# Kernel tuning notes

Measured on AMD Instinct MI355X. Metric: run time of the kernel, lower is better.

## Reference

```python
import jax, jax.numpy as jnp
import numpy as np

B, C, T, F = 4, 96, 320, 256
BN_EPS = 1e-5


def _cbp(x, W, b, gamma, beta, mean, var, a):
    """1x1 Conv2d + BatchNorm2d (inference stats) + PReLU (single param)."""
    y = jnp.einsum('oc,bctf->botf', W, x) + b[None, :, None, None]
    scale = gamma * jax.lax.rsqrt(var + BN_EPS)
    y = (y - mean[None, :, None, None]) * scale[None, :, None, None] + beta[None, :, None, None]
    return jnp.where(y >= 0, y, a * y)


def setup_inputs() -> dict:
    key = jax.random.key(0)
    ks = jax.random.split(key, 24)
    d = {"inp": jax.random.normal(ks[0], (B, C, T, F), dtype=jnp.float32)}

    def mk_params(i, cout):
        kk = jax.random.split(ks[i], 7)
        return dict(
            W=jax.random.normal(kk[0], (cout, C), dtype=jnp.float32) / np.sqrt(C),
            b=jnp.zeros((cout,), dtype=jnp.float32),
            gamma=jnp.ones((cout,), dtype=jnp.float32) + 0.1 * jax.random.normal(kk[1], (cout,), dtype=jnp.float32),
            beta=0.1 * jax.random.normal(kk[2], (cout,), dtype=jnp.float32),
            mean=0.1 * jax.random.normal(kk[3], (cout,), dtype=jnp.float32),
            var=jax.random.uniform(kk[4], (cout,), dtype=jnp.float32) + 0.5,
            a=jnp.float32(0.25),
        )

    for tag, i, cout in (("f", 1, 3 * C), ("t", 2, 2 * C), ("p", 3, C)):
        p = mk_params(i, cout)
        for k, v in p.items():
            d[k + "_" + tag] = v
    return d


def reference(inp,
              W_f, b_f, gamma_f, beta_f, mean_f, var_f, a_f,
              W_t, b_t, gamma_t, beta_t, mean_t, var_t, a_t,
              W_p, b_p, gamma_p, beta_p, mean_p, var_p, a_p):
    c = inp.shape[1]
    scale = 1.0 / jnp.sqrt(jnp.float32(c))

    # frequency-axis attention
    f_qkv = _cbp(inp, W_f, b_f, gamma_f, beta_f, mean_f, var_f, a_f)  # [B,3C,T,F]
    qf, kf, v = f_qkv[:, :c], f_qkv[:, c:2 * c], f_qkv[:, 2 * c:]
    f_score = jnp.einsum('bctf,bcty->btfy', qf, kf) * scale
    f_score = jax.nn.softmax(f_score, axis=-1)
    f_out = jnp.einsum('btfy,bcty->bctf', f_score, v)

    # time-axis attention (NOTE: original's masked_fill is non-inplace and
    # its result is discarded, so the causal mask has NO effect; replicated.)
    t_qk = _cbp(inp, W_t, b_t, gamma_t, beta_t, mean_t, var_t, a_t)  # [B,2C,T,F]
    qt, kt = t_qk[:, :c], t_qk[:, c:]
    t_score = jnp.einsum('bctf,bcyf->bfty', qt, kt) * scale
    t_score = jax.nn.softmax(t_score, axis=-1)
    t_out = jnp.einsum('bfty,bcyf->bctf', t_score, f_out)

    out = _cbp(t_out, W_p, b_p, gamma_p, beta_p, mean_p, var_p, a_p)
    return out + inp
```

## Files before the change

### kernel.cpp

```cpp
#include <hip/hip_runtime.h>
#include <math.h>

typedef float f4 __attribute__((ext_vector_type(4)));
typedef float f2 __attribute__((ext_vector_type(2)));
typedef float f32x4 __attribute__((ext_vector_type(4)));
typedef _Float16 h8 __attribute__((ext_vector_type(8)));

constexpr int B_ = 4, C_ = 96, T_ = 320, F_ = 256;
constexpr int TF_ = T_ * F_;
constexpr float EPS_ = 1e-5f;
constexpr size_t QH_ = (size_t)C_ * TF_;

constexpr int WHF = 0, WLF = 27648, WHT = 55296, WLT = 73728,
              WHP = 92160, WLP = 101376, WTOT = 110592;

__global__ __launch_bounds__(256)
void prep_kernel(const float* __restrict__ Wf, const float* __restrict__ Wt,
                 const float* __restrict__ Wp,
                 const float* __restrict__ bf, const float* __restrict__ gf,
                 const float* __restrict__ bef, const float* __restrict__ mf,
                 const float* __restrict__ vf,
                 const float* __restrict__ bt, const float* __restrict__ gt,
                 const float* __restrict__ bet, const float* __restrict__ mt,
                 const float* __restrict__ vt,
                 const float* __restrict__ bp, const float* __restrict__ gp,
                 const float* __restrict__ bep, const float* __restrict__ mp,
                 const float* __restrict__ vp,
                 _Float16* __restrict__ wsp, float* __restrict__ scsh)
{
    const int gtid = blockIdx.x * 256 + threadIdx.x;
    const int gsz  = gridDim.x * 256;
    for (int i = gtid; i < 27648; i += gsz) {
        const float w = Wf[i]; const _Float16 h = (_Float16)w;
        wsp[WHF + i] = h; wsp[WLF + i] = (_Float16)(w - (float)h);
    }
    for (int i = gtid; i < 18432; i += gsz) {
        const float w = Wt[i]; const _Float16 h = (_Float16)w;
        wsp[WHT + i] = h; wsp[WLT + i] = (_Float16)(w - (float)h);
    }
    for (int i = gtid; i < 9216; i += gsz) {
        const float w = Wp[i]; const _Float16 h = (_Float16)w;
        wsp[WHP + i] = h; wsp[WLP + i] = (_Float16)(w - (float)h);
    }
    if (gtid < 288) {
        const float sc = gf[gtid] * rsqrtf(vf[gtid] + EPS_);
        scsh[2 * gtid] = sc;
        scsh[2 * gtid + 1] = fmaf(bf[gtid] - mf[gtid], sc, bef[gtid]);
    } else if (gtid < 480) {
        const int i = gtid - 288;
        const float sc = gt[i] * rsqrtf(vt[i] + EPS_);
        scsh[576 + 2 * i] = sc;
        scsh[576 + 2 * i + 1] = fmaf(bt[i] - mt[i], sc, bet[i]);
    } else if (gtid < 576) {
        const int i = gtid - 480;
        const float sc = gp[i] * rsqrtf(vp[i] + EPS_);
        scsh[960 + 2 * i] = sc;
        scsh[960 + 2 * i + 1] = fmaf(bp[i] - mp[i], sc, bep[i]);
    }
}

__global__ __launch_bounds__(256, 3)
void conv_ft(const float* __restrict__ x, const _Float16* __restrict__ wsp,
             const float* __restrict__ scsh,
             const float* __restrict__ aPf, const float* __restrict__ aPt,
             _Float16* __restrict__ yf, _Float16* __restrict__ yt,
             int bsx, int bsyf, int bsyt)
{
    constexpr int LS = 200;
    extern __shared__ _Float16 ldsh[];
    _Float16* Xs = ldsh;

    x  += (size_t)blockIdx.y * bsx;
    yf += (size_t)blockIdx.y * bsyf;
    yt += (size_t)blockIdx.y * bsyt;

    const int tid = threadIdx.x;
    const int p0  = blockIdx.x * 64;

    const float* xg = x + p0;
    for (int e = tid; e < 64 * 12; e += 256) {
        const int p = e & 63, k0 = (e >> 6) * 8;
        const float* xp = xg + (size_t)k0 * TF_ + p;
        h8 hv, lv;
#pragma unroll
        for (int j = 0; j < 8; ++j) {
            const float xv = xp[(size_t)j * TF_];
            const _Float16 xh = (_Float16)xv;
            hv[j] = xh;
            lv[j] = (_Float16)(xv - (float)xh);
        }
        *(h8*)&Xs[p * LS + k0]      = hv;
        *(h8*)&Xs[p * LS + 96 + k0] = lv;
    }

    const int lane = tid & 63, wid = tid >> 6;
    const int l16 = lane & 15, lg = lane >> 4;
    const int wm = wid >> 1, wn = wid & 1;
    const float af_ = aPf[0], at_ = aPt[0];
    __syncthreads();

#pragma unroll 1
    for (int cg = 0; cg < 5; ++cg) {
        const _Float16 *Wh, *Wl; const float* ss; float a; _Float16* yo;
        if (cg < 3) {
            Wh = wsp + WHF + cg * 9216;  Wl = wsp + WLF + cg * 9216;
            ss = scsh + cg * 192;        a = af_;
            yo = yf + (size_t)cg * QH_;
        } else {
            const int c2 = cg - 3;
            Wh = wsp + WHT + c2 * 9216;  Wl = wsp + WLT + c2 * 9216;
            ss = scsh + 576 + c2 * 192;  a = at_;
            yo = yt + (size_t)c2 * QH_;
        }

        f32x4 acc[3][2];
#pragma unroll
        for (int m = 0; m < 3; ++m)
#pragma unroll
            for (int n = 0; n < 2; ++n) acc[m][n] = (f32x4){0.f, 0.f, 0.f, 0.f};

#pragma unroll
        for (int kk = 0; kk < 3; ++kk) {
            h8 bfh[2], bfl[2];
#pragma unroll
            for (int n = 0; n < 2; ++n) {
                const int prow = (wn * 2 + n) * 16 + l16;
                bfh[n] = *(const h8*)&Xs[prow * LS + kk * 32 + lg * 8];
                bfl[n] = *(const h8*)&Xs[prow * LS + 96 + kk * 32 + lg * 8];
            }
#pragma unroll
            for (int m = 0; m < 3; ++m) {
                const int row = (wm * 3 + m) * 16 + l16;
                const h8 wh = *(const h8*)&Wh[row * 96 + kk * 32 + lg * 8];
                const h8 wl = *(const h8*)&Wl[row * 96 + kk * 32 + lg * 8];
#pragma unroll
                for (int n = 0; n < 2; ++n) {
                    acc[m][n] = __builtin_amdgcn_mfma_f32_16x16x32_f16(wh, bfh[n], acc[m][n], 0, 0, 0);
                    acc[m][n] = __builtin_amdgcn_mfma_f32_16x16x32_f16(wl, bfh[n], acc[m][n], 0, 0, 0);
                    acc[m][n] = __builtin_amdgcn_mfma_f32_16x16x32_f16(wh, bfl[n], acc[m][n], 0, 0, 0);
                }
            }
        }

#pragma unroll
        for (int m = 0; m < 3; ++m) {
#pragma unroll
            for (int r = 0; r < 4; ++r) {
                const int col = (wm * 3 + m) * 16 + lg * 4 + r;
                const f2 sp = *(const f2*)&ss[2 * col];
                _Float16* yr = yo + (size_t)col * TF_ + p0 + wn * 32 + l16;
#pragma unroll
                for (int n = 0; n < 2; ++n) {
                    const float v = fmaf(acc[m][n][r], sp[0], sp[1]);
                    yr[n * 16] = (_Float16)(v >= 0.f ? v : a * v);
                }
            }
        }
    }
}

__global__ __launch_bounds__(256, 3)
void conv_p(const _Float16* __restrict__ x, const _Float16* __restrict__ wsp,
            const float* __restrict__ scsh, const float* __restrict__ aPp,
            _Float16* __restrict__ y, int bsx, int bsy)
{
    constexpr int LS = 104, PT = 160, NN = 5;
    extern __shared__ _Float16 ldsh[];
    _Float16* Xs = ldsh;

    x += (size_t)blockIdx.y * bsx;
    y += (size_t)blockIdx.y * bsy;

    const int tid = threadIdx.x;
    const int pt  = blockIdx.x & 1;
    const int g   = blockIdx.x >> 1;
    const int p0  = pt * PT;

    const _Float16* xg = x + (size_t)g * 96 * T_ + p0;
    for (int e = tid; e < PT * 12; e += 256) {
        const int p = e % PT, k0 = (e / PT) * 8;
        const _Float16* xp = xg + (size_t)k0 * T_ + p;
        h8 hv;
#pragma unroll
        for (int j = 0; j < 8; ++j) hv[j] = xp[(size_t)j * T_];
        *(h8*)&Xs[p * LS + k0] = hv;
    }

    const int lane = tid & 63, wid = tid >> 6;
    const int l16 = lane & 15, lg = lane >> 4;
    const int wm = wid >> 1, wn = wid & 1;
    const float a = aPp[0];
    const _Float16* Wh = wsp + WHP;
    const _Float16* Wl = wsp + WLP;
    const float* ss = scsh + 960;
    __syncthreads();

    f32x4 acc[3][NN];
#pragma unroll
    for (int m = 0; m < 3; ++m)
#pragma unroll
        for (int n = 0; n < NN; ++n) acc[m][n] = (f32x4){0.f, 0.f, 0.f, 0.f};

#pragma unroll
    for (int kk = 0; kk < 3; ++kk) {
        h8 bf[NN];
#pragma unroll
        for (int n = 0; n < NN; ++n)
            bf[n] = *(const h8*)&Xs[((wn * NN + n) * 16 + l16) * LS + kk * 32 + lg * 8];
#pragma unroll
        for (int m = 0; m < 3; ++m) {
            const int row = (wm * 3 + m) * 16 + l16;
            const h8 wh = *(const h8*)&Wh[row * 96 + kk * 32 + lg * 8];
            const h8 wl = *(const h8*)&Wl[row * 96 + kk * 32 + lg * 8];
#pragma unroll
            for (int n = 0; n < NN; ++n) {
                acc[m][n] = __builtin_amdgcn_mfma_f32_16x16x32_f16(wh, bf[n], acc[m][n], 0, 0, 0);
                acc[m][n] = __builtin_amdgcn_mfma_f32_16x16x32_f16(wl, bf[n], acc[m][n], 0, 0, 0);
            }
        }
    }

#pragma unroll
    for (int m = 0; m < 3; ++m) {
#pragma unroll
        for (int r = 0; r < 4; ++r) {
            const int col = (wm * 3 + m) * 16 + lg * 4 + r;
            const f2 sp = *(const f2*)&ss[2 * col];
            _Float16* yr = y + ((size_t)g * 96 + col) * T_ + p0 + wn * NN * 16 + l16;
#pragma unroll
            for (int n = 0; n < NN; ++n) {
                const float v = fmaf(acc[m][n][r], sp[0], sp[1]);
                yr[n * 16] = (_Float16)(v >= 0.f ? v : a * v);
            }
        }
    }
}

__global__ __launch_bounds__(256)
void transpose_h(const _Float16* __restrict__ in, _Float16* __restrict__ out,
                 int Mo, int No, int si, int so)
{
    __shared__ _Float16 tile[32][34];
    in  += (size_t)blockIdx.z * si;
    out += (size_t)blockIdx.z * so;
    const int n0 = blockIdx.x * 32, m0 = blockIdx.y * 32;
    const int tx = threadIdx.x, ty = threadIdx.y;
#pragma unroll
    for (int i = 0; i < 32; i += 8)
        tile[ty + i][tx] = in[(size_t)(n0 + ty + i) * Mo + (m0 + tx)];
    __syncthreads();
#pragma unroll
    for (int i = 0; i < 32; i += 8)
        out[(size_t)(m0 + ty + i) * No + (n0 + tx)] = tile[tx][ty + i];
}

__global__ __launch_bounds__(256)
void transpose_hf_res(const _Float16* __restrict__ in, const float* __restrict__ res,
                      float* __restrict__ out, int Mo, int No, int si, int sr, int so)
{
    __shared__ _Float16 tile[32][34];
    in  += (size_t)blockIdx.z * si;
    res += (size_t)blockIdx.z * sr;
    out += (size_t)blockIdx.z * so;
    const int n0 = blockIdx.x * 32, m0 = blockIdx.y * 32;
    const int tx = threadIdx.x, ty = threadIdx.y;
#pragma unroll
    for (int i = 0; i < 32; i += 8)
        tile[ty + i][tx] = in[(size_t)(n0 + ty + i) * Mo + (m0 + tx)];
    __syncthreads();
#pragma unroll
    for (int i = 0; i < 32; i += 8) {
        const size_t oidx = (size_t)(m0 + ty + i) * No + (n0 + tx);
        out[oidx] = (float)tile[tx][ty + i] + res[oidx];
    }
}

template<int MODE>
__global__ __launch_bounds__(256, 2)
void attn_mfma(const _Float16* __restrict__ Qb, const _Float16* __restrict__ Kb,
               const _Float16* __restrict__ Vb, _Float16* __restrict__ Ob,
               int qs, int ks, int vs, int os)
{
    constexpr int NY  = (MODE == 0) ? 256 : 320;
    constexpr int LD  = (MODE == 0) ? TF_ : T_;
    constexpr int NT  = NY / 16;
    constexpr int NYK = NY / 32;
    constexpr int KS  = 104;
    constexpr int VPS = NY + 24;
    constexpr int KVH = (NY * KS > 96 * VPS) ? NY * KS : 96 * VPS;
    constexpr int NG  = (MODE == 0) ? T_ : F_;
    constexpr int GOFF = (MODE == 0) ? F_ : C_ * T_;

    extern __shared__ _Float16 ldsh[];
    _Float16* KV = ldsh;
    _Float16* Pw = ldsh + KVH;

    const int lb    = blockIdx.y;
    const int strip = blockIdx.x / NG;
    const int grp   = blockIdx.x % NG;
    const int m0    = strip * 64;
    const size_t off = (size_t)grp * GOFF;
    const _Float16* Q = Qb + (size_t)lb * qs + off;
    const _Float16* K = Kb + (size_t)lb * ks + off;
    const _Float16* V = Vb + (size_t)lb * vs + off;
    _Float16*       O = Ob + (size_t)lb * os + off;

    const int tid  = threadIdx.x;
    const int lane = tid & 63, wid = tid >> 6;
    const int l16  = lane & 15, lg = lane >> 4;
    const int mw   = wid * 16;
    const float scale = 0.10206207261596575f;

    for (int e = tid; e < NY * 12; e += 256) {
        const int yy = e % NY, k0 = (e / NY) * 8;
        const _Float16* kp = K + (size_t)k0 * LD + yy;
        h8 hv;
#pragma unroll
        for (int j = 0; j < 8; ++j) hv[j] = kp[(size_t)j * LD];
        *(h8*)&KV[yy * KS + k0] = hv;
    }

    h8 aQ[3];
#pragma unroll
    for (int kk = 0; kk < 3; ++kk) {
        const _Float16* qp = Q + (size_t)(kk * 32 + lg * 8) * LD + m0 + mw + l16;
#pragma unroll
        for (int j = 0; j < 8; ++j) aQ[kk][j] = qp[(size_t)j * LD];
    }
    __syncthreads();

    f32x4 sacc[NT];
#pragma unroll
    for (int t = 0; t < NT; ++t) sacc[t] = (f32x4){0.f, 0.f, 0.f, 0.f};
#pragma unroll
    for (int kk = 0; kk < 3; ++kk) {
#pragma unroll
        for (int t = 0; t < NT; ++t) {
            const h8 bK = *(const h8*)&KV[(t * 16 + l16) * KS + kk * 32 + lg * 8];
            sacc[t] = __builtin_amdgcn_mfma_f32_16x16x32_f16(aQ[kk], bK, sacc[t], 0, 0, 0);
        }
    }

#pragma unroll
    for (int r = 0; r < 4; ++r) {
        float mx = sacc[0][r];
#pragma unroll
        for (int t = 1; t < NT; ++t) mx = fmaxf(mx, sacc[t][r]);
        for (int d = 1; d < 16; d <<= 1) mx = fmaxf(mx, __shfl_xor(mx, d));
        float pv[NT];
        float sum = 0.f;
#pragma unroll
        for (int t = 0; t < NT; ++t) {
            pv[t] = __expf((sacc[t][r] - mx) * scale); sum += pv[t];
        }
        for (int d = 1; d < 16; d <<= 1) sum += __shfl_xor(sum, d);
        const float inv = 1.f / sum;
#pragma unroll
        for (int t = 0; t < NT; ++t) sacc[t][r] = pv[t] * inv;
    }
    __syncthreads();

    constexpr int NY8 = NY / 8;
    for (int e = tid; e < 96 * NY8; e += 256) {
        const int c = e / NY8, y8 = e - c * NY8;
        *(h8*)&KV[c * VPS + y8 * 8] = *(const h8*)(V + (size_t)c * LD + y8 * 8);
    }
    __syncthreads();

    _Float16* Pme = Pw + wid * 640;
    f32x4 oacc[6];
#pragma unroll
    for (int ct = 0; ct < 6; ++ct) oacc[ct] = (f32x4){0.f, 0.f, 0.f, 0.f};

#pragma unroll
    for (int yk = 0; yk < NYK; ++yk) {
#pragma unroll
        for (int h = 0; h < 2; ++h)
#pragma unroll
            for (int r = 0; r < 4; ++r)
                Pme[(lg * 4 + r) * 40 + h * 16 + l16] = (_Float16)sacc[2 * yk + h][r];
        const h8 pf = *(const h8*)&Pme[l16 * 40 + lg * 8];
#pragma unroll
        for (int ct = 0; ct < 6; ++ct) {
            const h8 av = *(const h8*)&KV[(ct * 16 + l16) * VPS + yk * 32 + lg * 8];
            oacc[ct] = __builtin_amdgcn_mfma_f32_16x16x32_f16(av, pf, oacc[ct], 0, 0, 0);
        }
    }
#pragma unroll
    for (int ct = 0; ct < 6; ++ct)
#pragma unroll
        for (int r = 0; r < 4; ++r)
            O[(size_t)(ct * 16 + lg * 4 + r) * LD + m0 + mw + l16] = (_Float16)oacc[ct][r];
}

extern "C" void kernel_launch(void* const* d_in, const int* in_sizes, int n_in,
                              void* d_out, int out_size, void* d_ws, size_t ws_size,
                              hipStream_t stream)
{
    const float* inp = (const float*)d_in[0];
    const float* W_f = (const float*)d_in[1];  const float* b_f = (const float*)d_in[2];
    const float* g_f = (const float*)d_in[3];  const float* be_f = (const float*)d_in[4];
    const float* m_f = (const float*)d_in[5];  const float* v_f = (const float*)d_in[6];
    const float* a_f = (const float*)d_in[7];
    const float* W_t = (const float*)d_in[8];  const float* b_t = (const float*)d_in[9];
    const float* g_t = (const float*)d_in[10]; const float* be_t = (const float*)d_in[11];
    const float* m_t = (const float*)d_in[12]; const float* v_t = (const float*)d_in[13];
    const float* a_t = (const float*)d_in[14];
    const float* W_p = (const float*)d_in[15]; const float* b_p = (const float*)d_in[16];
    const float* g_p = (const float*)d_in[17]; const float* be_p = (const float*)d_in[18];
    const float* m_p = (const float*)d_in[19]; const float* v_p = (const float*)d_in[20];
    const float* a_p = (const float*)d_in[21];

    hipFuncSetAttribute((const void*)conv_ft,
                        hipFuncAttributeMaxDynamicSharedMemorySize, 25600);
    hipFuncSetAttribute((const void*)conv_p,
                        hipFuncAttributeMaxDynamicSharedMemorySize, 33280);
    hipFuncSetAttribute((const void*)attn_mfma<0>,
                        hipFuncAttributeMaxDynamicSharedMemorySize, 58880);
    hipFuncSetAttribute((const void*)attn_mfma<1>,
                        hipFuncAttributeMaxDynamicSharedMemorySize, 71680);

    constexpr int QH = (int)QH_;
    _Float16* wsh  = (_Float16*)d_ws;
    _Float16* wsp  = wsh + (size_t)6 * QH;
    float*    scsh = (float*)(wsh + (size_t)6 * QH + WTOT);

    prep_kernel<<<dim3(128), dim3(256), 0, stream>>>(
        W_f, W_t, W_p, b_f, g_f, be_f, m_f, v_f,
        b_t, g_t, be_t, m_t, v_t, b_p, g_p, be_p, m_p, v_p, wsp, scsh);

    for (int p = 0; p < 2; ++p) {
        const float* xb  = inp + (size_t)p * 2 * QH;
        float*       dob = (float*)d_out + (size_t)p * 2 * QH;
        _Float16*    doh = (_Float16*)dob;
        _Float16* fqkv  = wsh;
        _Float16* foutT = wsh + QH;
        _Float16* tqT   = wsh;
        _Float16* tkT   = wsh + (size_t)2 * QH;
        _Float16* tout  = wsh;
        _Float16* tmp   = wsh + (size_t)2 * QH;

        conv_ft<<<dim3(1280, 2), dim3(256), 25600, stream>>>(
            xb, wsp, scsh, a_f, a_t, fqkv, doh, QH, 3 * QH, 2 * QH);
        attn_mfma<0><<<dim3(T_ * (F_ / 64), 2), dim3(256), 58880, stream>>>(
            fqkv, fqkv + QH_, fqkv + 2 * QH_, fqkv, 3 * QH, 3 * QH, 3 * QH, 3 * QH);
        transpose_h<<<dim3(960, 8, 2), dim3(32, 8), 0, stream>>>(
            fqkv, foutT, F_, C_ * T_, 3 * QH, 3 * QH);
        transpose_h<<<dim3(960, 8, 2), dim3(32, 8), 0, stream>>>(
            doh, tqT, F_, C_ * T_, 2 * QH, 3 * QH);
        transpose_h<<<dim3(960, 8, 2), dim3(32, 8), 0, stream>>>(
            doh + QH_, tkT, F_, C_ * T_, 2 * QH, 3 * QH);
        attn_mfma<1><<<dim3(F_ * (T_ / 64), 2), dim3(256), 71680, stream>>>(
            tqT, tkT, foutT, tqT, 3 * QH, 3 * QH, 3 * QH, 3 * QH);
        conv_p<<<dim3(F_ * 2, 2), dim3(256), 33280, stream>>>(
            tout, wsp, scsh, a_p, tmp, 3 * QH, 3 * QH);
        transpose_hf_res<<<dim3(8, 960, 2), dim3(32, 8), 0, stream>>>(
            tmp, xb, dob, C_ * T_, F_, 3 * QH, QH, QH);
    }
}
```

Before: 720.3 us.

## Pipeline weight loads in conv_ft, merge transposes, batch four images when workspace allows

```diff
diff --git a/kernel.cpp b/kernel.cpp
--- a/kernel.cpp
+++ b/kernel.cpp
@@ -99,61 +99,91 @@
     const float af_ = aPf[0], at_ = aPt[0];
     __syncthreads();
 
-#pragma unroll 1
-    for (int cg = 0; cg < 5; ++cg) {
-        const _Float16 *Wh, *Wl; const float* ss; float a; _Float16* yo;
-        if (cg < 3) {
-            Wh = wsp + WHF + cg * 9216;  Wl = wsp + WLF + cg * 9216;
-            ss = scsh + cg * 192;        a = af_;
-            yo = yf + (size_t)cg * QH_;
-        } else {
-            const int c2 = cg - 3;
-            Wh = wsp + WHT + c2 * 9216;  Wl = wsp + WLT + c2 * 9216;
-            ss = scsh + 576 + c2 * 192;  a = at_;
-            yo = yt + (size_t)c2 * QH_;
-        }
-
-        f32x4 acc[3][2];
-#pragma unroll
-        for (int m = 0; m < 3; ++m)
-#pragma unroll
-            for (int n = 0; n < 2; ++n) acc[m][n] = (f32x4){0.f, 0.f, 0.f, 0.f};
-
-#pragma unroll
-        for (int kk = 0; kk < 3; ++kk) {
-            h8 bfh[2], bfl[2];
+    h8 xh[3][2], xl[3][2];
+#pragma unroll
+    for (int kk = 0; kk < 3; ++kk)
+#pragma unroll
+        for (int n = 0; n < 2; ++n) {
+            const int prow = (wn * 2 + n) * 16 + l16;
+            xh[kk][n] = *(const h8*)&Xs[prow * LS + kk * 32 + lg * 8];
+            xl[kk][n] = *(const h8*)&Xs[prow * LS + 96 + kk * 32 + lg * 8];
+        }
+
+    h8 wA[3], lA[3], wB[3], lB[3];
+    const int row0 = (wm * 3 + 0) * 16 + l16;
+    const int row1 = (wm * 3 + 1) * 16 + l16;
+    const int row2 = (wm * 3 + 2) * 16 + l16;
+    {
+        const _Float16* Wh = wsp + WHF;
+        const _Float16* Wl = wsp + WLF;
+        wA[0] = *(const h8*)&Wh[row0 * 96 + lg * 8];
+        wA[1] = *(const h8*)&Wh[row1 * 96 + lg * 8];
+        wA[2] = *(const h8*)&Wh[row2 * 96 + lg * 8];
+        lA[0] = *(const h8*)&Wl[row0 * 96 + lg * 8];
+        lA[1] = *(const h8*)&Wl[row1 * 96 + lg * 8];
+        lA[2] = *(const h8*)&Wl[row2 * 96 + lg * 8];
+    }
+
+    f32x4 acc[3][2];
+#pragma unroll
+    for (int m = 0; m < 3; ++m)
+#pragma unroll
+        for (int n = 0; n < 2; ++n) acc[m][n] = (f32x4){0.f, 0.f, 0.f, 0.f};
+
+#pragma unroll
+    for (int s = 0; s < 15; ++s) {
+        const int cg = s / 3, kk = s % 3;
+        if (s < 14) {
+            const int cg1 = (s + 1) / 3, kk1 = (s + 1) % 3;
+            const int wo = (cg1 < 3) ? (WHF + cg1 * 9216) : (WHT + (cg1 - 3) * 9216);
+            const int lo = (cg1 < 3) ? (WLF + cg1 * 9216) : (WLT + (cg1 - 3) * 9216);
+            const int eo = kk1 * 32 + lg * 8;
+            if (s & 1) {
+                wA[0] = *(const h8*)&wsp[wo + row0 * 96 + eo];
+                wA[1] = *(const h8*)&wsp[wo + row1 * 96 + eo];
+                wA[2] = *(const h8*)&wsp[wo + row2 * 96 + eo];
+                lA[0] = *(const h8*)&wsp[lo + row0 * 96 + eo];
+                lA[1] = *(const h8*)&wsp[lo + row1 * 96 + eo];
+                lA[2] = *(const h8*)&wsp[lo + row2 * 96 + eo];
+            } else {
+                wB[0] = *(const h8*)&wsp[wo + row0 * 96 + eo];
+                wB[1] = *(const h8*)&wsp[wo + row1 * 96 + eo];
+                wB[2] = *(const h8*)&wsp[wo + row2 * 96 + eo];
+                lB[0] = *(const h8*)&wsp[lo + row0 * 96 + eo];
+                lB[1] = *(const h8*)&wsp[lo + row1 * 96 + eo];
+                lB[2] = *(const h8*)&wsp[lo + row2 * 96 + eo];
+            }
+        }
+#pragma unroll
+        for (int m = 0; m < 3; ++m) {
+            const h8 wh = (s & 1) ? wB[m] : wA[m];
+            const h8 wl = (s & 1) ? lB[m] : lA[m];
 #pragma unroll
             for (int n = 0; n < 2; ++n) {
-                const int prow = (wn * 2 + n) * 16 + l16;
-                bfh[n] = *(const h8*)&Xs[prow * LS + kk * 32 + lg * 8];
-                bfl[n] = *(const h8*)&Xs[prow * LS + 96 + kk * 32 + lg * 8];
+                acc[m][n] = __builtin_amdgcn_mfma_f32_16x16x32_f16(wh, xh[kk][n], acc[m][n], 0, 0, 0);
+                acc[m][n] = __builtin_amdgcn_mfma_f32_16x16x32_f16(wl, xh[kk][n], acc[m][n], 0, 0, 0);
+                acc[m][n] = __builtin_amdgcn_mfma_f32_16x16x32_f16(wh, xl[kk][n], acc[m][n], 0, 0, 0);
             }
+        }
+        if (kk == 2) {
+            const float* ss = (cg < 3) ? scsh + cg * 192 : scsh + 576 + (cg - 3) * 192;
+            const float a   = (cg < 3) ? af_ : at_;
+            _Float16* yo = (cg < 3) ? yf + (size_t)cg * QH_ : yt + (size_t)(cg - 3) * QH_;
 #pragma unroll
             for (int m = 0; m < 3; ++m) {
-                const int row = (wm * 3 + m) * 16 + l16;
-                const h8 wh = *(const h8*)&Wh[row * 96 + kk * 32 + lg * 8];
-                const h8 wl = *(const h8*)&Wl[row * 96 + kk * 32 + lg * 8];
-#pragma unroll
-                for (int n = 0; n < 2; ++n) {
-                    acc[m][n] = __builtin_amdgcn_mfma_f32_16x16x32_f16(wh, bfh[n], acc[m][n], 0, 0, 0);
-                    acc[m][n] = __builtin_amdgcn_mfma_f32_16x16x32_f16(wl, bfh[n], acc[m][n], 0, 0, 0);
-                    acc[m][n] = __builtin_amdgcn_mfma_f32_16x16x32_f16(wh, bfl[n], acc[m][n], 0, 0, 0);
+#pragma unroll
+                for (int r = 0; r < 4; ++r) {
+                    const int col = (wm * 3 + m) * 16 + lg * 4 + r;
+                    const f2 sp = *(const f2*)&ss[2 * col];
+                    _Float16* yr = yo + (size_t)col * TF_ + p0 + wn * 32 + l16;
+#pragma unroll
+                    for (int n = 0; n < 2; ++n) {
+                        const float v = fmaf(acc[m][n][r], sp[0], sp[1]);
+                        yr[n * 16] = (_Float16)(v >= 0.f ? v : a * v);
+                    }
                 }
-            }
-        }
-
-#pragma unroll
-        for (int m = 0; m < 3; ++m) {
-#pragma unroll
-            for (int r = 0; r < 4; ++r) {
-                const int col = (wm * 3 + m) * 16 + lg * 4 + r;
-                const f2 sp = *(const f2*)&ss[2 * col];
-                _Float16* yr = yo + (size_t)col * TF_ + p0 + wn * 32 + l16;
-#pragma unroll
-                for (int n = 0; n < 2; ++n) {
-                    const float v = fmaf(acc[m][n][r], sp[0], sp[1]);
-                    yr[n * 16] = (_Float16)(v >= 0.f ? v : a * v);
-                }
+#pragma unroll
+                for (int n = 0; n < 2; ++n) acc[m][n] = (f32x4){0.f, 0.f, 0.f, 0.f};
             }
         }
     }
@@ -237,21 +267,41 @@
 }
 
 __global__ __launch_bounds__(256)
-void transpose_h(const _Float16* __restrict__ in, _Float16* __restrict__ out,
-                 int Mo, int No, int si, int so)
-{
+void transpose_trA(const _Float16* __restrict__ doh, _Float16* __restrict__ wsh)
+{
+    const int b = blockIdx.z >> 1, t = blockIdx.z & 1;
+    const _Float16* in  = t ? doh + (size_t)b * 2 * QH_
+                            : wsh + (size_t)b * 3 * QH_;
+    _Float16*       out = t ? wsh + (size_t)b * 3 * QH_ + 2 * QH_
+                            : wsh + (size_t)b * 3 * QH_ + QH_;
     __shared__ _Float16 tile[32][34];
-    in  += (size_t)blockIdx.z * si;
-    out += (size_t)blockIdx.z * so;
     const int n0 = blockIdx.x * 32, m0 = blockIdx.y * 32;
     const int tx = threadIdx.x, ty = threadIdx.y;
 #pragma unroll
     for (int i = 0; i < 32; i += 8)
-        tile[ty + i][tx] = in[(size_t)(n0 + ty + i) * Mo + (m0 + tx)];
+        tile[ty + i][tx] = in[(size_t)(n0 + ty + i) * F_ + (m0 + tx)];
     __syncthreads();
 #pragma unroll
     for (int i = 0; i < 32; i += 8)
-        out[(size_t)(m0 + ty + i) * No + (n0 + tx)] = tile[tx][ty + i];
+        out[(size_t)(m0 + ty + i) * (C_ * T_) + (n0 + tx)] = tile[tx][ty + i];
+}
+
+__global__ __launch_bounds__(256)
+void transpose_trB(const _Float16* __restrict__ doh, _Float16* __restrict__ wsh)
+{
+    const int b = blockIdx.z;
+    const _Float16* in  = doh + (size_t)b * 2 * QH_ + QH_;
+    _Float16*       out = wsh + (size_t)b * 3 * QH_;
+    __shared__ _Float16 tile[32][34];
+    const int n0 = blockIdx.x * 32, m0 = blockIdx.y * 32;
+    const int tx = threadIdx.x, ty = threadIdx.y;
+#pragma unroll
+    for (int i = 0; i < 32; i += 8)
+        tile[ty + i][tx] = in[(size_t)(n0 + ty + i) * F_ + (m0 + tx)];
+    __syncthreads();
+#pragma unroll
+    for (int i = 0; i < 32; i += 8)
+        out[(size_t)(m0 + ty + i) * (C_ * T_) + (n0 + tx)] = tile[tx][ty + i];
 }
 
 __global__ __launch_bounds__(256)
@@ -421,40 +471,34 @@
                         hipFuncAttributeMaxDynamicSharedMemorySize, 71680);
 
     constexpr int QH = (int)QH_;
+    const size_t need4 = (size_t)12 * QH * 2 + (size_t)WTOT * 2 + 1152 * 4 + 4096;
+    const int G = (ws_size >= need4) ? 4 : 2;
+
     _Float16* wsh  = (_Float16*)d_ws;
-    _Float16* wsp  = wsh + (size_t)6 * QH;
-    float*    scsh = (float*)(wsh + (size_t)6 * QH + WTOT);
+    _Float16* wsp  = wsh + (size_t)3 * G * QH;
+    float*    scsh = (float*)(wsp + WTOT);
 
     prep_kernel<<<dim3(128), dim3(256), 0, stream>>>(
         W_f, W_t, W_p, b_f, g_f, be_f, m_f, v_f,
         b_t, g_t, be_t, m_t, v_t, b_p, g_p, be_p, m_p, v_p, wsp, scsh);
 
-    for (int p = 0; p < 2; ++p) {
-        const float* xb  = inp + (size_t)p * 2 * QH;
-        float*       dob = (float*)d_out + (size_t)p * 2 * QH;
+    for (int p = 0; p < B_ / G; ++p) {
+        const float* xb  = inp + (size_t)p * G * QH;
+        float*       dob = (float*)d_out + (size_t)p * G * QH;
         _Float16*    doh = (_Float16*)dob;
-        _Float16* fqkv  = wsh;
-        _Float16* foutT = wsh + QH;
-        _Float16* tqT   = wsh;
-        _Float16* tkT   = wsh + (size_t)2 * QH;
-        _Float16* tout  = wsh;
-        _Float16* tmp   = wsh + (size_t)2 * QH;
-
-        conv_ft<<<dim3(1280, 2), dim3(256), 25600, stream>>>(
-            xb, wsp, scsh, a_f, a_t, fqkv, doh, QH, 3 * QH, 2 * QH);
-        attn_mfma<0><<<dim3(T_ * (F_ / 64), 2), dim3(256), 58880, stream>>>(
-            fqkv, fqkv + QH_, fqkv + 2 * QH_, fqkv, 3 * QH, 3 * QH, 3 * QH, 3 * QH);
-        transpose_h<<<dim3(960, 8, 2), dim3(32, 8), 0, stream>>>(
-            fqkv, foutT, F_, C_ * T_, 3 * QH, 3 * QH);
-        transpose_h<<<dim3(960, 8, 2), dim3(32, 8), 0, stream>>>(
-            doh, tqT, F_, C_ * T_, 2 * QH, 3 * QH);
-        transpose_h<<<dim3(960, 8, 2), dim3(32, 8), 0, stream>>>(
-            doh + QH_, tkT, F_, C_ * T_, 2 * QH, 3 * QH);
-        attn_mfma<1><<<dim3(F_ * (T_ / 64), 2), dim3(256), 71680, stream>>>(
-            tqT, tkT, foutT, tqT, 3 * QH, 3 * QH, 3 * QH, 3 * QH);
-        conv_p<<<dim3(F_ * 2, 2), dim3(256), 33280, stream>>>(
-            tout, wsp, scsh, a_p, tmp, 3 * QH, 3 * QH);
-        transpose_hf_res<<<dim3(8, 960, 2), dim3(32, 8), 0, stream>>>(
-            tmp, xb, dob, C_ * T_, F_, 3 * QH, QH, QH);
-    }
-}
+
+        conv_ft<<<dim3(1280, G), dim3(256), 25600, stream>>>(
+            xb, wsp, scsh, a_f, a_t, wsh, doh, QH, 3 * QH, 2 * QH);
+        attn_mfma<0><<<dim3(T_ * (F_ / 64), G), dim3(256), 58880, stream>>>(
+            wsh, wsh + QH_, wsh + 2 * QH_, wsh, 3 * QH, 3 * QH, 3 * QH, 3 * QH);
+        transpose_trA<<<dim3(960, 8, 2 * G), dim3(32, 8), 0, stream>>>(doh, wsh);
+        transpose_trB<<<dim3(960, 8, G), dim3(32, 8), 0, stream>>>(doh, wsh);
+        attn_mfma<1><<<dim3(F_ * (T_ / 64), G), dim3(256), 71680, stream>>>(
+            wsh + 2 * QH_, wsh, wsh + QH_, wsh + 2 * QH_,
+            3 * QH, 3 * QH, 3 * QH, 3 * QH);
+        conv_p<<<dim3(F_ * 2, G), dim3(256), 33280, stream>>>(
+            wsh + 2 * QH_, wsp, scsh, a_p, wsh, 3 * QH, 3 * QH);
+        transpose_hf_res<<<dim3(8, 960, G), dim3(32, 8), 0, stream>>>(
+            wsh, xb, dob, C_ * T_, F_, 3 * QH, QH, QH);
+    }
+}
```

Measured after the change: 868.2 us. +20.5%, slower.
